# Performance work log

Hardware: AMD Instinct MI355X
Metric: run time of the kernel (lower is better)

The kernel has to match this reference:

```python
import jax, jax.numpy as jnp
import numpy as np

N_BLOCKS = 64
BLOCK_R = 128  # rows per block (output features per block)
BLOCK_C = 128  # cols per block (input features per block)
BATCH = 4096

def setup_inputs() -> dict:
    key = jax.random.key(0)
    k1, k2 = jax.random.split(key)
    x = jax.random.normal(k1, (BATCH, N_BLOCKS * BLOCK_C), dtype=jnp.float32)
    # learned parameters: diagonal blocks, torch.randn init
    blocks = jax.random.normal(k2, (N_BLOCKS, BLOCK_R, BLOCK_C), dtype=jnp.float32)
    return {"x": x, "blocks": blocks}

def reference(x, blocks):
    # Equivalent to x @ full_matrix.T where full_matrix = blockdiag(blocks),
    # but computed directly on the blocks (no zero-fill materialization).
    B = x.shape[0]
    n, r, c = blocks.shape
    xb = x.reshape(B, n, c)                      # split input into per-block column slices
    out = jnp.einsum('bnc,nrc->bnr', xb, blocks)  # per-block GEMM: x_slice @ block.T
    return out.reshape(B, n * r)
```

## Files before the change

### kernel.cpp

```cpp
#include <hip/hip_runtime.h>
#include <hip/hip_bf16.h>


typedef __bf16 bf16_8 __attribute__((ext_vector_type(8)));
typedef __bf16 bf16_4 __attribute__((ext_vector_type(4)));
typedef float f32x4 __attribute__((ext_vector_type(4)));

__global__ __launch_bounds__(512, 4)
void BlocDiagLinear_kernel(const float* __restrict__ x,
                           const float* __restrict__ blocks,
                           float* __restrict__ out)
{
    __shared__ __align__(16) __bf16 ws[128 * 128];

    const int bid = blockIdx.x;
    const int nb  = bid & 63;
    const int mt  = bid >> 6;

    const int t    = threadIdx.x;
    const int lane = t & 63;
    const int w    = t >> 6;
    const int lm   = lane & 15;
    const int q    = lane >> 4;

    const float* xb = x + (size_t)(mt * 128 + w * 16 + lm) * 8192
                        + (size_t)nb * 128 + q * 8;
    float4 raw[8];
#pragma unroll
    for (int kk = 0; kk < 4; ++kk) {
        raw[2 * kk]     = *(const float4*)(xb + kk * 32);
        raw[2 * kk + 1] = *(const float4*)(xb + kk * 32 + 4);
    }

    const int c4 = t & 31;
    const int r0 = t >> 5;
    const float* wg = blocks + (size_t)nb * 16384;
    char* wsb = (char*)ws;
#pragma unroll
    for (int i = 0; i < 8; ++i) {
        const int row = i * 16 + r0;
        const float4 vw = *(const float4*)(wg + row * 128 + c4 * 4);
        bf16_4 bw = { (__bf16)vw.x, (__bf16)vw.y, (__bf16)vw.z, (__bf16)vw.w };
        *(bf16_4*)(wsb + ((row * 256 + c4 * 8) ^ ((r0 & 7) << 4))) = bw;
    }
    __syncthreads();

    bf16_8 b[4];
#pragma unroll
    for (int kk = 0; kk < 4; ++kk) {
        const float4 lo = raw[2 * kk];
        const float4 hi = raw[2 * kk + 1];
        b[kk] = (bf16_8){ (__bf16)lo.x, (__bf16)lo.y, (__bf16)lo.z, (__bf16)lo.w,
                          (__bf16)hi.x, (__bf16)hi.y, (__bf16)hi.z, (__bf16)hi.w };
    }

    f32x4 acc[8];
#pragma unroll
    for (int mi = 0; mi < 8; ++mi)
        acc[mi] = (f32x4){0.f, 0.f, 0.f, 0.f};

    const int swz = (lm & 7) << 4;

#pragma unroll
    for (int kk = 0; kk < 4; ++kk) {
        bf16_8 a[8];
#pragma unroll
        for (int mi = 0; mi < 8; ++mi) {
            const int byte = ((mi * 16 + lm) * 256 + kk * 64 + q * 16) ^ swz;
            a[mi] = *(const bf16_8*)(wsb + byte);
        }
#pragma unroll
        for (int mi = 0; mi < 8; ++mi)
            acc[mi] = __builtin_amdgcn_mfma_f32_16x16x32_bf16(
                          a[mi], b[kk], acc[mi], 0, 0, 0);
    }

    float* og = out + (size_t)(mt * 128 + w * 16 + lm) * 8192
                    + (size_t)nb * 128 + q * 4;
#pragma unroll
    for (int mi = 0; mi < 8; ++mi)
        *(f32x4*)(og + mi * 16) = acc[mi];
}

extern "C" void kernel_launch(void* const* d_in, const int* in_sizes, int n_in,
                              void* d_out, int out_size, void* d_ws, size_t ws_size,
                              hipStream_t stream) {
    const float* x      = (const float*)d_in[0];
    const float* blocks = (const float*)d_in[1];
    float* out          = (float*)d_out;
    BlocDiagLinear_kernel<<<dim3(64 * 32), dim3(512), 0, stream>>>(x, blocks, out);
}
```

Measured before the change: 234.3 us.

## Reuse weight block across four M-tiles with prefetched x loads; pad LDS

Each workgroup now processes four 128-row batch tiles for one diagonal block. The block is converted to bf16 in LDS once and reused across all four tiles, and the next tile's x rows are prefetched into registers while the current tile computes. This cuts redundant weight loads and conversions fourfold and shrinks the grid from 2048 to 512 workgroups. The XOR swizzle in LDS is replaced by a padded row stride of 136. Fewer workgroups may leave the GPU less fully occupied, and the padded stride changes the LDS bank-conflict pattern.

```diff
diff --git a/kernel.cpp b/kernel.cpp
--- a/kernel.cpp
+++ b/kernel.cpp
@@ -6,16 +6,18 @@
 typedef __bf16 bf16_4 __attribute__((ext_vector_type(4)));
 typedef float f32x4 __attribute__((ext_vector_type(4)));
 
+#define LDS_K 136
+
 __global__ __launch_bounds__(512, 4)
 void BlocDiagLinear_kernel(const float* __restrict__ x,
                            const float* __restrict__ blocks,
                            float* __restrict__ out)
 {
-    __shared__ __align__(16) __bf16 ws[128 * 128];
+    __shared__ __align__(16) __bf16 ws[128 * LDS_K];
 
     const int bid = blockIdx.x;
     const int nb  = bid & 63;
-    const int mt  = bid >> 6;
+    const int wgm = bid >> 6;
 
     const int t    = threadIdx.x;
     const int lane = t & 63;
@@ -23,63 +25,72 @@
     const int lm   = lane & 15;
     const int q    = lane >> 4;
 
-    const float* xb = x + (size_t)(mt * 128 + w * 16 + lm) * 8192
+    const float* xp = x + (size_t)(wgm * 4 * 128 + w * 16 + lm) * 8192
                         + (size_t)nb * 128 + q * 8;
     float4 raw[8];
 #pragma unroll
     for (int kk = 0; kk < 4; ++kk) {
-        raw[2 * kk]     = *(const float4*)(xb + kk * 32);
-        raw[2 * kk + 1] = *(const float4*)(xb + kk * 32 + 4);
+        raw[2 * kk]     = *(const float4*)(xp + kk * 32);
+        raw[2 * kk + 1] = *(const float4*)(xp + kk * 32 + 4);
     }
 
     const int c4 = t & 31;
     const int r0 = t >> 5;
     const float* wg = blocks + (size_t)nb * 16384;
-    char* wsb = (char*)ws;
 #pragma unroll
     for (int i = 0; i < 8; ++i) {
         const int row = i * 16 + r0;
         const float4 vw = *(const float4*)(wg + row * 128 + c4 * 4);
         bf16_4 bw = { (__bf16)vw.x, (__bf16)vw.y, (__bf16)vw.z, (__bf16)vw.w };
-        *(bf16_4*)(wsb + ((row * 256 + c4 * 8) ^ ((r0 & 7) << 4))) = bw;
+        *(bf16_4*)(ws + row * LDS_K + c4 * 4) = bw;
     }
     __syncthreads();
 
-    bf16_8 b[4];
+    float* op = out + (size_t)(wgm * 4 * 128 + w * 16 + lm) * 8192
+                    + (size_t)nb * 128 + q * 4;
+
+#pragma unroll 1
+    for (int it = 0; it < 4; ++it) {
+        bf16_8 b[4];
 #pragma unroll
-    for (int kk = 0; kk < 4; ++kk) {
-        const float4 lo = raw[2 * kk];
-        const float4 hi = raw[2 * kk + 1];
-        b[kk] = (bf16_8){ (__bf16)lo.x, (__bf16)lo.y, (__bf16)lo.z, (__bf16)lo.w,
-                          (__bf16)hi.x, (__bf16)hi.y, (__bf16)hi.z, (__bf16)hi.w };
-    }
+        for (int kk = 0; kk < 4; ++kk) {
+            const float4 lo = raw[2 * kk];
+            const float4 hi = raw[2 * kk + 1];
+            b[kk] = (bf16_8){ (__bf16)lo.x, (__bf16)lo.y, (__bf16)lo.z, (__bf16)lo.w,
+                              (__bf16)hi.x, (__bf16)hi.y, (__bf16)hi.z, (__bf16)hi.w };
+        }
+        if (it < 3) {
+            const float* pn = xp + (size_t)(it + 1) * 128 * 8192;
+#pragma unroll
+            for (int kk = 0; kk < 4; ++kk) {
+                raw[2 * kk]     = *(const float4*)(pn + kk * 32);
+                raw[2 * kk + 1] = *(const float4*)(pn + kk * 32 + 4);
+            }
+        }
 
-    f32x4 acc[8];
+        f32x4 acc[8];
 #pragma unroll
-    for (int mi = 0; mi < 8; ++mi)
-        acc[mi] = (f32x4){0.f, 0.f, 0.f, 0.f};
-
-    const int swz = (lm & 7) << 4;
+        for (int mi = 0; mi < 8; ++mi)
+            acc[mi] = (f32x4){0.f, 0.f, 0.f, 0.f};
 
 #pragma unroll
-    for (int kk = 0; kk < 4; ++kk) {
-        bf16_8 a[8];
+        for (int kk = 0; kk < 4; ++kk) {
+            bf16_8 a[8];
 #pragma unroll
-        for (int mi = 0; mi < 8; ++mi) {
-            const int byte = ((mi * 16 + lm) * 256 + kk * 64 + q * 16) ^ swz;
-            a[mi] = *(const bf16_8*)(wsb + byte);
+            for (int mi = 0; mi < 8; ++mi)
+                a[mi] = *(const bf16_8*)(ws + (mi * 16 + lm) * LDS_K
+                                            + kk * 32 + q * 8);
+#pragma unroll
+            for (int mi = 0; mi < 8; ++mi)
+                acc[mi] = __builtin_amdgcn_mfma_f32_16x16x32_bf16(
+                              a[mi], b[kk], acc[mi], 0, 0, 0);
         }
+
+        float* og = op + (size_t)it * 128 * 8192;
 #pragma unroll
         for (int mi = 0; mi < 8; ++mi)
-            acc[mi] = __builtin_amdgcn_mfma_f32_16x16x32_bf16(
-                          a[mi], b[kk], acc[mi], 0, 0, 0);
+            *(f32x4*)(og + mi * 16) = acc[mi];
     }
-
-    float* og = out + (size_t)(mt * 128 + w * 16 + lm) * 8192
-                    + (size_t)nb * 128 + q * 4;
-#pragma unroll
-    for (int mi = 0; mi < 8; ++mi)
-        *(f32x4*)(og + mi * 16) = acc[mi];
 }
 
 extern "C" void kernel_launch(void* const* d_in, const int* in_sizes, int n_in,
@@ -88,5 +99,5 @@
     const float* x      = (const float*)d_in[0];
     const float* blocks = (const float*)d_in[1];
     float* out          = (float*)d_out;
-    BlocDiagLinear_kernel<<<dim3(64 * 32), dim3(512), 0, stream>>>(x, blocks, out);
+    BlocDiagLinear_kernel<<<dim3(64 * 8), dim3(512), 0, stream>>>(x, blocks, out);
 }
```

After: 295.9 us. 26.3% more time.

## Persistent per-block tiles with double-buffered async x loads into LDS

Applied to the files above, without the earlier changes.

Each workgroup now processes 512 batch rows for one diagonal block, looping over 16 chunks of 32 rows, so the weight block is converted to bf16 and staged in LDS once per workgroup instead of four times. The x tile is streamed into LDS with global_load_lds into a double buffer, which overlaps loading the next chunks with the MFMA work on the current one. The weight LDS layout switches from an XOR swizzle to a padded row stride. The grid drops to 512 workgroups, which lowers parallelism. The loop also adds two barriers per chunk and issues fewer MFMAs per wave between them.

```diff
diff --git a/kernel.cpp b/kernel.cpp
--- a/kernel.cpp
+++ b/kernel.cpp
@@ -6,16 +6,19 @@
 typedef __bf16 bf16_4 __attribute__((ext_vector_type(4)));
 typedef float f32x4 __attribute__((ext_vector_type(4)));
 
+#define LDS_WK 136
+
 __global__ __launch_bounds__(512, 4)
 void BlocDiagLinear_kernel(const float* __restrict__ x,
                            const float* __restrict__ blocks,
                            float* __restrict__ out)
 {
-    __shared__ __align__(16) __bf16 ws[128 * 128];
+    __shared__ __align__(16) __bf16 wlds[128 * LDS_WK];
+    __shared__ __align__(16) float  xlds[2][32 * 128];
 
     const int bid = blockIdx.x;
     const int nb  = bid & 63;
-    const int mt  = bid >> 6;
+    const int own = bid >> 6;
 
     const int t    = threadIdx.x;
     const int lane = t & 63;
@@ -23,63 +26,93 @@
     const int lm   = lane & 15;
     const int q    = lane >> 4;
 
-    const float* xb = x + (size_t)(mt * 128 + w * 16 + lm) * 8192
-                        + (size_t)nb * 128 + q * 8;
-    float4 raw[8];
-#pragma unroll
-    for (int kk = 0; kk < 4; ++kk) {
-        raw[2 * kk]     = *(const float4*)(xb + kk * 32);
-        raw[2 * kk + 1] = *(const float4*)(xb + kk * 32 + 4);
+    const int bg   = w & 1;
+    const int rb   = w >> 1;
+
+    const int l5  = lane >> 5;
+    const int p31 = lane & 31;
+
+#define STAGE(bufi, ch)                                                       \
+    {                                                                         \
+        _Pragma("unroll")                                                     \
+        for (int i = 0; i < 2; ++i) {                                         \
+            const int row  = w * 4 + i * 2 + l5;                              \
+            const int gcol = (p31 ^ (row & 7)) * 4;                           \
+            const float* src = x + (size_t)(own * 512 + (ch) * 32 + row) * 8192 \
+                                 + nb * 128 + gcol;                           \
+            __builtin_amdgcn_global_load_lds(                                 \
+                (const __attribute__((address_space(1))) unsigned int*)src,   \
+                (__attribute__((address_space(3))) unsigned int*)             \
+                    (&xlds[bufi][(w * 4 + i * 2) * 128]),                     \
+                16, 0, 0);                                                    \
+        }                                                                     \
     }
 
     const int c4 = t & 31;
     const int r0 = t >> 5;
     const float* wg = blocks + (size_t)nb * 16384;
-    char* wsb = (char*)ws;
+    float4 wraw[8];
+#pragma unroll
+    for (int i = 0; i < 8; ++i)
+        wraw[i] = *(const float4*)(wg + (i * 16 + r0) * 128 + c4 * 4);
+
+    STAGE(0, 0);
+    STAGE(1, 1);
+
 #pragma unroll
     for (int i = 0; i < 8; ++i) {
         const int row = i * 16 + r0;
-        const float4 vw = *(const float4*)(wg + row * 128 + c4 * 4);
-        bf16_4 bw = { (__bf16)vw.x, (__bf16)vw.y, (__bf16)vw.z, (__bf16)vw.w };
-        *(bf16_4*)(wsb + ((row * 256 + c4 * 8) ^ ((r0 & 7) << 4))) = bw;
+        bf16_4 bw = { (__bf16)wraw[i].x, (__bf16)wraw[i].y,
+                      (__bf16)wraw[i].z, (__bf16)wraw[i].w };
+        *(bf16_4*)(wlds + row * LDS_WK + c4 * 4) = bw;
     }
-    __syncthreads();
+    asm volatile("s_waitcnt lgkmcnt(0)" ::: "memory");
+    __builtin_amdgcn_sched_barrier(0);
+    __builtin_amdgcn_s_barrier();
 
-    bf16_8 b[4];
-#pragma unroll
-    for (int kk = 0; kk < 4; ++kk) {
-        const float4 lo = raw[2 * kk];
-        const float4 hi = raw[2 * kk + 1];
-        b[kk] = (bf16_8){ (__bf16)lo.x, (__bf16)lo.y, (__bf16)lo.z, (__bf16)lo.w,
-                          (__bf16)hi.x, (__bf16)hi.y, (__bf16)hi.z, (__bf16)hi.w };
-    }
+#pragma unroll 1
+    for (int ch = 0; ch < 16; ++ch) {
+        const int cur = ch & 1;
 
-    f32x4 acc[8];
-#pragma unroll
-    for (int mi = 0; mi < 8; ++mi)
-        acc[mi] = (f32x4){0.f, 0.f, 0.f, 0.f};
+        asm volatile("s_waitcnt vmcnt(2)" ::: "memory");
+        __builtin_amdgcn_sched_barrier(0);
+        __builtin_amdgcn_s_barrier();
+        __builtin_amdgcn_sched_barrier(0);
 
-    const int swz = (lm & 7) << 4;
+        f32x4 acc[2];
+        acc[0] = (f32x4){0.f, 0.f, 0.f, 0.f};
+        acc[1] = (f32x4){0.f, 0.f, 0.f, 0.f};
+
+        const int xrow = bg * 16 + lm;
+        const int s    = xrow & 7;
+        const float* xr = &xlds[cur][xrow * 128];
 
 #pragma unroll
-    for (int kk = 0; kk < 4; ++kk) {
-        bf16_8 a[8];
+        for (int kk = 0; kk < 4; ++kk) {
+            const f32x4 lo = *(const f32x4*)(xr + (kk * 8 + ((q * 2 + 0) ^ s)) * 4);
+            const f32x4 hi = *(const f32x4*)(xr + (kk * 8 + ((q * 2 + 1) ^ s)) * 4);
+            const bf16_8 b = { (__bf16)lo.x, (__bf16)lo.y, (__bf16)lo.z, (__bf16)lo.w,
+                               (__bf16)hi.x, (__bf16)hi.y, (__bf16)hi.z, (__bf16)hi.w };
 #pragma unroll
-        for (int mi = 0; mi < 8; ++mi) {
-            const int byte = ((mi * 16 + lm) * 256 + kk * 64 + q * 16) ^ swz;
-            a[mi] = *(const bf16_8*)(wsb + byte);
+            for (int rg = 0; rg < 2; ++rg) {
+                const bf16_8 a = *(const bf16_8*)(wlds + (rb * 32 + rg * 16 + lm) * LDS_WK
+                                                      + kk * 32 + q * 8);
+                acc[rg] = __builtin_amdgcn_mfma_f32_16x16x32_bf16(a, b, acc[rg], 0, 0, 0);
+            }
         }
-#pragma unroll
-        for (int mi = 0; mi < 8; ++mi)
-            acc[mi] = __builtin_amdgcn_mfma_f32_16x16x32_bf16(
-                          a[mi], b[kk], acc[mi], 0, 0, 0);
+
+        float* og = out + (size_t)(own * 512 + ch * 32 + bg * 16 + lm) * 8192
+                        + nb * 128 + rb * 32 + q * 4;
+        *(f32x4*)(og)      = acc[0];
+        *(f32x4*)(og + 16) = acc[1];
+
+        __builtin_amdgcn_sched_barrier(0);
+        __builtin_amdgcn_s_barrier();
+        __builtin_amdgcn_sched_barrier(0);
+
+        if (ch + 2 < 16) STAGE(cur, ch + 2);
     }
-
-    float* og = out + (size_t)(mt * 128 + w * 16 + lm) * 8192
-                    + (size_t)nb * 128 + q * 4;
-#pragma unroll
-    for (int mi = 0; mi < 8; ++mi)
-        *(f32x4*)(og + mi * 16) = acc[mi];
+#undef STAGE
 }
 
 extern "C" void kernel_launch(void* const* d_in, const int* in_sizes, int n_in,
@@ -88,5 +121,5 @@
     const float* x      = (const float*)d_in[0];
     const float* blocks = (const float*)d_in[1];
     float* out          = (float*)d_out;
-    BlocDiagLinear_kernel<<<dim3(64 * 32), dim3(512), 0, stream>>>(x, blocks, out);
+    BlocDiagLinear_kernel<<<dim3(64 * 8), dim3(512), 0, stream>>>(x, blocks, out);
 }
```

Result: no change. 232.9 us (-0.6%).
